# Kernel optimization log

Measured on AMD Instinct MI355X. Metric: run time of the kernel, lower is better.

## Reference

```python
import jax, jax.numpy as jnp
import numpy as np

WIN = (2, 4, 4)
SHIFT = (1, 2, 2)
NUM_HEADS = 8
LN_EPS = 1e-5


def _rel_pos_index(ws):
    wt, wh, ww = ws
    coords = np.stack(np.meshgrid(np.arange(wt), np.arange(wh), np.arange(ww), indexing='ij'))
    cf = coords.reshape(3, -1)                      # [3, N]
    rel = cf[:, :, None] - cf[:, None, :]           # [3, N, N]
    rel = rel.transpose(1, 2, 0).copy()             # [N, N, 3]
    rel[..., 0] += wt - 1
    rel[..., 1] += wh - 1
    rel[..., 2] += ww - 1
    rel[..., 0] *= (2 * wh - 1) * (2 * ww - 1)
    rel[..., 1] *= 2 * ww - 1
    return rel.sum(-1)                              # [N, N] int

REL_IDX = _rel_pos_index(WIN)


def _layer_norm(x, w, b):
    mu = jnp.mean(x, axis=-1, keepdims=True)
    var = jnp.mean(jnp.square(x - mu), axis=-1, keepdims=True)
    return (x - mu) * jax.lax.rsqrt(var + LN_EPS) * w + b


def setup_inputs() -> dict:
    key = jax.random.key(0)
    ks = jax.random.split(key, 8)
    C, Cm = 256, 1024
    inp = {
        'x': jax.random.normal(ks[0], (2, 16, 64, 64, C), jnp.float32),
        'norm1_w': jnp.ones((C,), jnp.float32),
        'norm1_b': jnp.zeros((C,), jnp.float32),
        'qkv_w': jax.random.normal(ks[1], (C, 3 * C), jnp.float32) * 0.02,
        'qkv_b': jnp.zeros((3 * C,), jnp.float32),
        'proj_w': jax.random.normal(ks[2], (C, C), jnp.float32) * 0.02,
        'proj_b': jnp.zeros((C,), jnp.float32),
        'rel_bias_table': jax.random.normal(ks[3], (147, NUM_HEADS), jnp.float32) * 0.02,
        'norm2_w': jnp.ones((C,), jnp.float32),
        'norm2_b': jnp.zeros((C,), jnp.float32),
        'mlp_w1': jax.random.normal(ks[4], (C, Cm), jnp.float32) * 0.02,
        'mlp_b1': jnp.zeros((Cm,), jnp.float32),
        'mlp_w2': jax.random.normal(ks[5], (Cm, C), jnp.float32) * 0.02,
        'mlp_b2': jnp.zeros((C,), jnp.float32),
    }
    return inp


def reference(x, norm1_w, norm1_b, qkv_w, qkv_b, proj_w, proj_b,
              rel_bias_table, norm2_w, norm2_b, mlp_w1, mlp_b1, mlp_w2, mlp_b2):
    B, T, H, W, C = x.shape
    wT, wH, wW = WIN
    nh = NUM_HEADS
    d = C // nh
    scale = d ** (-0.5)
    N = wT * wH * wW

    shortcut = x
    h = _layer_norm(x, norm1_w, norm1_b)
    # cyclic shift (no attention mask is applied in the original block)
    h = jnp.roll(h, shift=(-SHIFT[0], -SHIFT[1], -SHIFT[2]), axis=(1, 2, 3))
    # window partition -> [B*nW, N, C]
    h = h.reshape(B, T // wT, wT, H // wH, wH, W // wW, wW, C)
    h = h.transpose(0, 1, 3, 5, 2, 4, 6, 7).reshape(-1, N, C)
    B_ = h.shape[0]

    qkv = (h @ qkv_w + qkv_b).reshape(B_, N, 3, nh, d).transpose(2, 0, 3, 1, 4)
    q, k, v = qkv[0] * scale, qkv[1], qkv[2]          # [B_, nh, N, d]
    attn = jnp.einsum('bhnd,bhmd->bhnm', q, k)        # [B_, nh, N, N]
    bias = rel_bias_table[REL_IDX].transpose(2, 0, 1)  # [nh, N, N]
    attn = jax.nn.softmax(attn + bias[None], axis=-1)
    o = jnp.einsum('bhnm,bhmd->bhnd', attn, v)
    o = o.transpose(0, 2, 1, 3).reshape(B_, N, C)
    o = o @ proj_w + proj_b

    # window reverse -> [B, T, H, W, C]
    o = o.reshape(B, T // wT, H // wH, W // wW, wT, wH, wW, C)
    o = o.transpose(0, 1, 4, 2, 5, 3, 6, 7).reshape(B, T, H, W, C)
    o = jnp.roll(o, shift=SHIFT, axis=(1, 2, 3))

    x = shortcut + o
    m = _layer_norm(x, norm2_w, norm2_b)
    m = jax.nn.gelu(m @ mlp_w1 + mlp_b1, approximate=False) @ mlp_w2 + mlp_b2
    return x + m
```

## Files before the change

kernel.cpp:

```cpp
#include <hip/hip_runtime.h>
#include <hip/hip_bf16.h>
#include <cstdint>
#include <cstddef>

typedef __attribute__((ext_vector_type(8)))  short  s16x8;
typedef __attribute__((ext_vector_type(4)))  float  fp32x4;
typedef __attribute__((ext_vector_type(16))) float  fp32x16;
typedef __attribute__((ext_vector_type(4)))  unsigned short u16x4;

static __device__ __forceinline__ unsigned short f2bf(float f) {
    __hip_bfloat16 h = __float2bfloat16(f);
    return __builtin_bit_cast(unsigned short, h);
}

static __device__ __forceinline__ fp32x16 mfma32(s16x8 a, s16x8 b, fp32x16 c) {
    return __builtin_amdgcn_mfma_f32_32x32x16_bf16(a, b, c, 0, 0, 0);
}
static __device__ __forceinline__ fp32x4 mfma16(s16x8 a, s16x8 b, fp32x4 c) {
    return __builtin_amdgcn_mfma_f32_16x16x32_bf16(a, b, c, 0, 0, 0);
}

static __device__ __forceinline__ float wave_sum(float v) {
#pragma unroll
    for (int off = 32; off > 0; off >>= 1) v += __shfl_xor(v, off, 64);
    return v;
}

static __device__ __forceinline__ float gelu_f(float u) {
    float t = u * (1.0f + 0.044715f * u * u) * 1.595769122f;
    return u * (1.0f / (1.0f + __expf(-t)));
}

#define NTOK   131072
#define CDIM   256

__global__ void prep_kernel(const float* __restrict__ qkv_w, const float* __restrict__ proj_w,
                            const float* __restrict__ w1,    const float* __restrict__ w2,
                            const float* __restrict__ rel,
                            unsigned short* __restrict__ qkvT, unsigned short* __restrict__ projT,
                            unsigned short* __restrict__ w1T,  unsigned short* __restrict__ w2T,
                            float* __restrict__ btab) {
    int id = blockIdx.x * 256 + threadIdx.x;
    if (id < 196608) {
        int n = id >> 8, k = id & 255;
        qkvT[id] = f2bf(qkv_w[k * 768 + n]);
    } else if (id < 262144) {
        int e = id - 196608; int n = e >> 8, k = e & 255;
        projT[e] = f2bf(proj_w[k * 256 + n]);
    } else if (id < 524288) {
        int e = id - 262144; int n = e >> 8, k = e & 255;
        w1T[e] = f2bf(w1[k * 1024 + n]);
    } else if (id < 786432) {
        int e = id - 524288; int n = e >> 10, k = e & 1023;
        w2T[e] = f2bf(w2[k * 256 + n]);
    } else {
        int e = id - 786432;
        int h = e >> 10, rem = e & 1023, n = rem >> 5, m = rem & 31;
        int tn = n >> 4, hn = (n >> 2) & 3, wn = n & 3;
        int tm = m >> 4, hm = (m >> 2) & 3, wm = m & 3;
        int ridx = (tn - tm + 1) * 49 + (hn - hm + 3) * 7 + (wn - wm + 3);
        btab[e] = rel[ridx * 8 + h];
    }
}

__global__ __launch_bounds__(256) void ln_kernel(const float* __restrict__ in,
                                                 const float* __restrict__ w,
                                                 const float* __restrict__ b,
                                                 unsigned short* __restrict__ out) {
    int tid = threadIdx.x, lane = tid & 63, wid = tid >> 6;
    long r = (long)blockIdx.x * 4 + wid;
    int n = (int)(r & 31); int win = (int)(r >> 5);
    int b_ = win >> 11, tw = (win >> 8) & 7, hw = (win >> 4) & 15, ww = win & 15;
    int ti = n >> 4, hi = (n >> 2) & 3, wi = n & 3;
    int t = tw * 2 + ti, hh = hw * 4 + hi, wv = ww * 4 + wi;
    int ts = (t + 1) & 15, hs = (hh + 2) & 63, wsd = (wv + 2) & 63;
    long src = ((long)((b_ * 16 + ts) * 64 + hs)) * 64 + wsd;

    float4 v = *(const float4*)&in[src * CDIM + lane * 4];
    float vv[4] = {v.x, v.y, v.z, v.w};
    float s = vv[0] + vv[1] + vv[2] + vv[3];
    s = wave_sum(s);
    float mean = s * (1.0f / 256.0f);
    float q = vv[0]*vv[0] + vv[1]*vv[1] + vv[2]*vv[2] + vv[3]*vv[3];
    q = wave_sum(q);
    float var = q * (1.0f / 256.0f) - mean * mean;
    float rstd = rsqrtf(var + 1e-5f);
    int c0 = lane * 4;
    u16x4 o;
#pragma unroll
    for (int j = 0; j < 4; ++j)
        o[j] = f2bf((vv[j] - mean) * rstd * w[c0 + j] + b[c0 + j]);
    *(u16x4*)&out[r * CDIM + c0] = o;
}

template <int K, int EPI, int NS, int NX>
__global__ __launch_bounds__(256, 2) void gemm128(const unsigned short* __restrict__ A,
                                                  const unsigned short* __restrict__ Bt,
                                                  const float* __restrict__ bias,
                                                  float* __restrict__ outf,
                                                  unsigned short* __restrict__ outb) {
    __shared__ unsigned short lds[32768];
    const int tid = threadIdx.x;
    const int lane = tid & 63, wid = tid >> 6;
    const int wm = wid >> 1, wn = wid & 1;
    constexpr int NWG = 1024 * NX;
    constexpr int CPX = NWG / 8;
    const int bid = blockIdx.x;
    const int wg = (bid & 7) * CPX + (bid >> 3);
    const int n0 = (wg % NX) * 128;
    const size_t m0 = (size_t)(wg / NX) * 128;
    constexpr int NK = K / 64;

    fp32x4 acc[4][4] = {};

    const unsigned short* gA[4];
    const unsigned short* gB[4];
    int ldst[4];
#pragma unroll
    for (int i = 0; i < 4; ++i) {
        int L = i * 256 + tid;
        int r = L >> 3, c = L & 7;
        int sc = c ^ (r & 7);
        gA[i] = A  + (m0 + r) * (size_t)K + sc * 8;
        gB[i] = Bt + (size_t)(n0 + r) * K + sc * 8;
        ldst[i] = L * 8;
    }
    auto stage = [&](int buf) {
#pragma unroll
        for (int i = 0; i < 4; ++i) {
            __builtin_amdgcn_global_load_lds(
                (const __attribute__((address_space(1))) void*)gA[i],
                (__attribute__((address_space(3))) void*)(lds + buf * 16384 + ldst[i]),
                16, 0, 0);
            __builtin_amdgcn_global_load_lds(
                (const __attribute__((address_space(1))) void*)gB[i],
                (__attribute__((address_space(3))) void*)(lds + buf * 16384 + 8192 + ldst[i]),
                16, 0, 0);
            gA[i] += 64; gB[i] += 64;
        }
    };

    const int r7 = (lane & 15) & 7;
    const int aoff = (wm * 64 + (lane & 15)) * 64 + (((lane >> 4) ^ r7) << 3);
    const int boff = 8192 + (wn * 64 + (lane & 15)) * 64 + (((lane >> 4) ^ r7) << 3);

    stage(0);
    for (int kt = 0; kt < NK; ++kt) {
        __syncthreads();
        if (kt + 1 < NK) stage((kt + 1) & 1);
        const int cb = (kt & 1) * 16384;
#pragma unroll
        for (int ks = 0; ks < 2; ++ks) {
            const int kx = ks * 32;
            s16x8 a[4], b[4];
#pragma unroll
            for (int m = 0; m < 4; ++m)
                a[m] = *(const s16x8*)(lds + cb + (aoff ^ kx) + m * 1024);
#pragma unroll
            for (int n = 0; n < 4; ++n)
                b[n] = *(const s16x8*)(lds + cb + (boff ^ kx) + n * 1024);
#pragma unroll
            for (int m = 0; m < 4; ++m)
#pragma unroll
                for (int n = 0; n < 4; ++n)
                    acc[m][n] = mfma16(a[m], b[n], acc[m][n]);
        }
    }

    float bv[4];
#pragma unroll
    for (int n = 0; n < 4; ++n) bv[n] = bias[n0 + wn * 64 + n * 16 + (lane & 15)];

#pragma unroll
    for (int m = 0; m < 4; ++m) {
#pragma unroll
        for (int rg = 0; rg < 4; ++rg) {
            size_t gr = m0 + wm * 64 + m * 16 + ((lane >> 4) << 2) + rg;
#pragma unroll
            for (int n = 0; n < 4; ++n) {
                int gc = n0 + wn * 64 + n * 16 + (lane & 15);
                float v = acc[m][n][rg] + bv[n];
                if (EPI == 0) {
                    outb[gr * NS + gc] = f2bf(v);
                } else if (EPI == 2) {
                    outb[gr * NS + gc] = f2bf(gelu_f(v));
                } else {
                    outf[gr * NS + gc] += v;
                }
            }
        }
    }
}

template <int K>
__global__ __launch_bounds__(512) void gemm256_proj(const unsigned short* __restrict__ A,
                                                    const unsigned short* __restrict__ Bt,
                                                    const float* __restrict__ bias,
                                                    float* __restrict__ outf,
                                                    unsigned short* __restrict__ outb,
                                                    const float* __restrict__ resid,
                                                    const float* __restrict__ lnw,
                                                    const float* __restrict__ lnb) {
    extern __shared__ unsigned short lds[];
    const int tid = threadIdx.x;
    const int lane = tid & 63, wid = tid >> 6;
    const int wm = wid >> 2, wn = wid & 3;
    const int bid = blockIdx.x;
    const int wg = (bid & 7) * 64 + (bid >> 3);
    const size_t m0 = (size_t)wg * 256;
    constexpr int NK = K / 64;

    fp32x4 acc[8][4] = {};

    auto stage = [&](int kt, int buf) {
#pragma unroll
        for (int i = 0; i < 4; ++i) {
            int L = i * 512 + tid;
            int r = L >> 3, c = L & 7;
            int sc = c ^ (r & 7);
            const unsigned short* ga = A + (m0 + r) * K + kt * 64 + sc * 8;
            __builtin_amdgcn_global_load_lds(
                (const __attribute__((address_space(1))) void*)ga,
                (__attribute__((address_space(3))) void*)(lds + buf * 16384 + L * 8),
                16, 0, 0);
            const unsigned short* gb = Bt + (size_t)r * K + kt * 64 + sc * 8;
            __builtin_amdgcn_global_load_lds(
                (const __attribute__((address_space(1))) void*)gb,
                (__attribute__((address_space(3))) void*)(lds + 32768 + buf * 16384 + L * 8),
                16, 0, 0);
        }
    };

    stage(0, 0);
    for (int kt = 0; kt < NK; ++kt) {
        __syncthreads();
        if (kt + 1 < NK) stage(kt + 1, (kt + 1) & 1);
        const unsigned short* As = lds + (kt & 1) * 16384;
        const unsigned short* Bs = lds + 32768 + (kt & 1) * 16384;
#pragma unroll
        for (int q = 0; q < 4; ++q) {
            const int qm = q >> 1, qn = q & 1;
            s16x8 a[4][2], b[2][2];
#pragma unroll
            for (int m = 0; m < 4; ++m)
#pragma unroll
                for (int ks = 0; ks < 2; ++ks) {
                    int row = wm * 128 + qm * 64 + m * 16 + (lane & 15);
                    int j = ks * 4 + (lane >> 4);
                    a[m][ks] = *(const s16x8*)(As + row * 64 + ((j ^ (row & 7)) << 3));
                }
#pragma unroll
            for (int n = 0; n < 2; ++n)
#pragma unroll
                for (int ks = 0; ks < 2; ++ks) {
                    int row = wn * 64 + qn * 32 + n * 16 + (lane & 15);
                    int j = ks * 4 + (lane >> 4);
                    b[n][ks] = *(const s16x8*)(Bs + row * 64 + ((j ^ (row & 7)) << 3));
                }
#pragma unroll
            for (int ks = 0; ks < 2; ++ks)
#pragma unroll
                for (int m = 0; m < 4; ++m)
#pragma unroll
                    for (int n = 0; n < 2; ++n)
                        acc[qm * 4 + m][qn * 2 + n] =
                            mfma16(a[m][ks], b[n][ks], acc[qm * 4 + m][qn * 2 + n]);
        }
        __syncthreads();
    }

    float bv[4];
#pragma unroll
    for (int n = 0; n < 4; ++n) bv[n] = bias[wn * 64 + n * 16 + (lane & 15)];

    float* part = (float*)lds;
    float lw[4], lb[4];
#pragma unroll
    for (int n = 0; n < 4; ++n) {
        int gc = wn * 64 + n * 16 + (lane & 15);
        lw[n] = lnw[gc]; lb[n] = lnb[gc];
    }
#pragma unroll
    for (int m = 0; m < 8; ++m) {
#pragma unroll
        for (int rg = 0; rg < 4; ++rg) {
            int row_t = wm * 128 + m * 16 + ((lane >> 4) << 2) + rg;
            size_t gr = m0 + row_t;
            int win = (int)(gr >> 5), n_ = (int)(gr & 31);
            int b_ = win >> 11, tw = (win >> 8) & 7, hw = (win >> 4) & 15, ww = win & 15;
            int ti = n_ >> 4, hi = (n_ >> 2) & 3, wi = n_ & 3;
            int t = tw * 2 + ti, hh = hw * 4 + hi, wv = ww * 4 + wi;
            int ts = (t + 1) & 15, hs = (hh + 2) & 63, wsd = (wv + 2) & 63;
            size_t dst = ((size_t)((b_ * 16 + ts) * 64 + hs)) * 64 + wsd;
            float s = 0.f, q = 0.f;
#pragma unroll
            for (int n = 0; n < 4; ++n) {
                int gc = wn * 64 + n * 16 + (lane & 15);
                float v = acc[m][n][rg] + bv[n] + resid[dst * CDIM + gc];
                outf[dst * CDIM + gc] = v;
                acc[m][n][rg] = v;
                s += v; q += v * v;
            }
#pragma unroll
            for (int off = 1; off < 16; off <<= 1) {
                s += __shfl_xor(s, off, 16);
                q += __shfl_xor(q, off, 16);
            }
            if ((lane & 15) == 0) {
                part[(row_t * 4 + wn) * 2]     = s;
                part[(row_t * 4 + wn) * 2 + 1] = q;
            }
        }
    }
    __syncthreads();
#pragma unroll
    for (int m = 0; m < 8; ++m) {
#pragma unroll
        for (int rg = 0; rg < 4; ++rg) {
            int row_t = wm * 128 + m * 16 + ((lane >> 4) << 2) + rg;
            size_t gr = m0 + row_t;
            int win = (int)(gr >> 5), n_ = (int)(gr & 31);
            int b_ = win >> 11, tw = (win >> 8) & 7, hw = (win >> 4) & 15, ww = win & 15;
            int ti = n_ >> 4, hi = (n_ >> 2) & 3, wi = n_ & 3;
            int t = tw * 2 + ti, hh = hw * 4 + hi, wv = ww * 4 + wi;
            int ts = (t + 1) & 15, hs = (hh + 2) & 63, wsd = (wv + 2) & 63;
            size_t dst = ((size_t)((b_ * 16 + ts) * 64 + hs)) * 64 + wsd;
            float4 p0 = *(const float4*)&part[row_t * 8];
            float4 p1 = *(const float4*)&part[row_t * 8 + 4];
            float s = p0.x + p0.z + p1.x + p1.z;
            float q = p0.y + p0.w + p1.y + p1.w;
            float mean = s * (1.0f / 256.0f);
            float var  = q * (1.0f / 256.0f) - mean * mean;
            float rstd = rsqrtf(var + 1e-5f);
#pragma unroll
            for (int n = 0; n < 4; ++n) {
                int gc = wn * 64 + n * 16 + (lane & 15);
                float v = acc[m][n][rg];
                outb[dst * CDIM + gc] = f2bf((v - mean) * rstd * lw[n] + lb[n]);
            }
        }
    }
}

__global__ __launch_bounds__(256) void attn_kernel(const unsigned short* __restrict__ qkv,
                                                   const float* __restrict__ btab,
                                                   unsigned short* __restrict__ obuf) {
    __shared__ unsigned short sP[4][1280];
    __shared__ unsigned short sVt[4][1280];
    int tid = threadIdx.x, lane = tid & 63, wid = tid >> 6;
    int task = blockIdx.x * 4 + wid;
    int win = task >> 3, hh = task & 7;
    const unsigned short* base = qkv + (size_t)win * 32 * 768 + hh * 32;
    int q = lane & 31, h = lane >> 5;

    s16x8 v0 = *(const s16x8*)(base + 512 + q * 768 + h * 16);
    s16x8 v1 = *(const s16x8*)(base + 512 + q * 768 + h * 16 + 8);
#pragma unroll
    for (int j = 0; j < 8; ++j) {
        sVt[wid][(h * 16 + j) * 40 + q]     = (unsigned short)v0[j];
        sVt[wid][(h * 16 + 8 + j) * 40 + q] = (unsigned short)v1[j];
    }

    s16x8 aq0 = *(const s16x8*)(base + q * 768 + h * 8);
    s16x8 aq1 = *(const s16x8*)(base + q * 768 + 16 + h * 8);
    s16x8 bk0 = *(const s16x8*)(base + 256 + q * 768 + h * 8);
    s16x8 bk1 = *(const s16x8*)(base + 256 + q * 768 + 16 + h * 8);
    fp32x16 S = {0.0f};
    S = mfma32(aq0, bk0, S);
    S = mfma32(aq1, bk1, S);

    const float scale = 0.17677669529663687f;
    float pr[16];
#pragma unroll
    for (int r = 0; r < 16; ++r) {
        int row = (r & 3) + 8 * (r >> 2) + 4 * h;
        pr[r] = S[r] * scale + btab[(hh * 32 + row) * 32 + q];
    }
#pragma unroll
    for (int r = 0; r < 16; ++r) {
        float mx = pr[r];
#pragma unroll
        for (int off = 16; off > 0; off >>= 1) mx = fmaxf(mx, __shfl_xor(mx, off, 64));
        float e = __expf(pr[r] - mx);
        float sm = e;
#pragma unroll
        for (int off = 16; off > 0; off >>= 1) sm += __shfl_xor(sm, off, 64);
        pr[r] = e * __builtin_amdgcn_rcpf(sm);
    }
#pragma unroll
    for (int r = 0; r < 16; ++r) {
        int row = (r & 3) + 8 * (r >> 2) + 4 * h;
        sP[wid][row * 40 + q] = f2bf(pr[r]);
    }
    __syncthreads();

    s16x8 pa0 = *(const s16x8*)&sP[wid][q * 40 + h * 8];
    s16x8 pa1 = *(const s16x8*)&sP[wid][q * 40 + 16 + h * 8];
    s16x8 vb0 = *(const s16x8*)&sVt[wid][q * 40 + h * 8];
    s16x8 vb1 = *(const s16x8*)&sVt[wid][q * 40 + 16 + h * 8];
    fp32x16 O = {0.0f};
    O = mfma32(pa0, vb0, O);
    O = mfma32(pa1, vb1, O);
#pragma unroll
    for (int r = 0; r < 16; ++r) {
        int row = (r & 3) + 8 * (r >> 2) + 4 * h;
        obuf[((size_t)win * 32 + row) * 256 + hh * 32 + q] = f2bf(O[r]);
    }
}

extern "C" void kernel_launch(void* const* d_in, const int* in_sizes, int n_in,
                              void* d_out, int out_size, void* d_ws, size_t ws_size,
                              hipStream_t stream) {
    const float* x      = (const float*)d_in[0];
    const float* n1w    = (const float*)d_in[1];
    const float* n1b    = (const float*)d_in[2];
    const float* qkv_w  = (const float*)d_in[3];
    const float* qkv_b  = (const float*)d_in[4];
    const float* proj_w = (const float*)d_in[5];
    const float* proj_b = (const float*)d_in[6];
    const float* rel    = (const float*)d_in[7];
    const float* n2w    = (const float*)d_in[8];
    const float* n2b    = (const float*)d_in[9];
    const float* w1     = (const float*)d_in[10];
    const float* b1     = (const float*)d_in[11];
    const float* w2     = (const float*)d_in[12];
    const float* b2     = (const float*)d_in[13];
    float* out = (float*)d_out;

    char* ws = (char*)d_ws;
    unsigned short* hwin = (unsigned short*)ws;
    unsigned short* big  = (unsigned short*)(ws + 67108864);
    unsigned short* obuf = big + 100663296;
    char* wreg = ws + 67108864 + 268435456;
    unsigned short* qkvT  = (unsigned short*)(wreg);
    unsigned short* projT = (unsigned short*)(wreg + 393216);
    unsigned short* w1T   = (unsigned short*)(wreg + 524288);
    unsigned short* w2T   = (unsigned short*)(wreg + 1048576);
    float*          btab  = (float*)(wreg + 1572864);

    prep_kernel<<<3104, 256, 0, stream>>>(qkv_w, proj_w, w1, w2, rel, qkvT, projT, w1T, w2T, btab);

    ln_kernel<<<NTOK / 4, 256, 0, stream>>>(x, n1w, n1b, hwin);

    gemm128<256, 0, 768, 6><<<6144, 256, 0, stream>>>(hwin, qkvT, qkv_b, nullptr, big);

    attn_kernel<<<8192, 256, 0, stream>>>(big, btab, obuf);

    gemm256_proj<256><<<512, 512, 131072, stream>>>(obuf, projT, proj_b, out, hwin, x, n2w, n2b);

    gemm128<256, 2, 1024, 8><<<8192, 256, 0, stream>>>(hwin, w1T, b1, nullptr, big);

    gemm128<1024, 3, 256, 2><<<2048, 256, 0, stream>>>(big, w2T, b2, out, nullptr);
}
```

Measured before the change: 685.4 us.

## Shrink gemm128 K-tile to 32 and halve LDS to raise occupancy

The 128x128 bf16 GEMM now stages K-slices of 32 instead of 64, which halves the double-buffered LDS footprint to 32 KB. It raises the launch-bounds occupancy hint from 2 to 4 blocks per CU. The LDS swizzle is replaced with a rotation-based scheme sized for 4 chunks per row, and the K loop is fully unrolled. In exchange there are twice as many barriers and stage issues per unit of K, with less MFMA work between each sync, and register pressure must fit the tighter occupancy bound.

```diff
diff --git a/kernel.cpp b/kernel.cpp
--- a/kernel.cpp
+++ b/kernel.cpp
@@ -94,12 +94,12 @@
 }
 
 template <int K, int EPI, int NS, int NX>
-__global__ __launch_bounds__(256, 2) void gemm128(const unsigned short* __restrict__ A,
+__global__ __launch_bounds__(256, 4) void gemm128(const unsigned short* __restrict__ A,
                                                   const unsigned short* __restrict__ Bt,
                                                   const float* __restrict__ bias,
                                                   float* __restrict__ outf,
                                                   unsigned short* __restrict__ outb) {
-    __shared__ unsigned short lds[32768];
+    __shared__ unsigned short lds[16384];
     const int tid = threadIdx.x;
     const int lane = tid & 63, wid = tid >> 6;
     const int wm = wid >> 1, wn = wid & 1;
@@ -109,67 +109,71 @@
     const int wg = (bid & 7) * CPX + (bid >> 3);
     const int n0 = (wg % NX) * 128;
     const size_t m0 = (size_t)(wg / NX) * 128;
-    constexpr int NK = K / 64;
+    constexpr int NK = K / 32;
 
     fp32x4 acc[4][4] = {};
 
-    const unsigned short* gA[4];
-    const unsigned short* gB[4];
-    int ldst[4];
-#pragma unroll
-    for (int i = 0; i < 4; ++i) {
+    const unsigned short* gAp[2];
+    const unsigned short* gBp[2];
+    int dOff[2];
+#pragma unroll
+    for (int i = 0; i < 2; ++i) {
         int L = i * 256 + tid;
-        int r = L >> 3, c = L & 7;
-        int sc = c ^ (r & 7);
-        gA[i] = A  + (m0 + r) * (size_t)K + sc * 8;
-        gB[i] = Bt + (size_t)(n0 + r) * K + sc * 8;
-        ldst[i] = L * 8;
-    }
-    auto stage = [&](int buf) {
-#pragma unroll
-        for (int i = 0; i < 4; ++i) {
-            __builtin_amdgcn_global_load_lds(
-                (const __attribute__((address_space(1))) void*)gA[i],
-                (__attribute__((address_space(3))) void*)(lds + buf * 16384 + ldst[i]),
-                16, 0, 0);
-            __builtin_amdgcn_global_load_lds(
-                (const __attribute__((address_space(1))) void*)gB[i],
-                (__attribute__((address_space(3))) void*)(lds + buf * 16384 + 8192 + ldst[i]),
-                16, 0, 0);
-            gA[i] += 64; gB[i] += 64;
-        }
-    };
-
-    const int r7 = (lane & 15) & 7;
-    const int aoff = (wm * 64 + (lane & 15)) * 64 + (((lane >> 4) ^ r7) << 3);
-    const int boff = 8192 + (wn * 64 + (lane & 15)) * 64 + (((lane >> 4) ^ r7) << 3);
-
-    stage(0);
+        int r = L >> 2, cp = L & 3;
+        int j = (cp - (r >> 1)) & 3;
+        gAp[i] = A  + (m0 + r) * (size_t)K + j * 8;
+        gBp[i] = Bt + (size_t)(n0 + r) * K + j * 8;
+        dOff[i] = L * 8;
+    }
+
+    const int l15 = lane & 15, jj = lane >> 4;
+    const int sig = (jj + (l15 >> 1)) & 3;
+    const int aread = (wm * 64 + l15) * 32 + sig * 8;
+    const int bread = 4096 + (wn * 64 + l15) * 32 + sig * 8;
+
+#pragma unroll
+    for (int i = 0; i < 2; ++i) {
+        __builtin_amdgcn_global_load_lds(
+            (const __attribute__((address_space(1))) void*)gAp[i],
+            (__attribute__((address_space(3))) void*)(lds + dOff[i]), 16, 0, 0);
+        __builtin_amdgcn_global_load_lds(
+            (const __attribute__((address_space(1))) void*)gBp[i],
+            (__attribute__((address_space(3))) void*)(lds + 4096 + dOff[i]), 16, 0, 0);
+    }
+
+#pragma unroll
     for (int kt = 0; kt < NK; ++kt) {
         __syncthreads();
-        if (kt + 1 < NK) stage((kt + 1) & 1);
-        const int cb = (kt & 1) * 16384;
-#pragma unroll
-        for (int ks = 0; ks < 2; ++ks) {
-            const int kx = ks * 32;
-            s16x8 a[4], b[4];
-#pragma unroll
-            for (int m = 0; m < 4; ++m)
-                a[m] = *(const s16x8*)(lds + cb + (aoff ^ kx) + m * 1024);
+        if (kt + 1 < NK) {
+            const int nb = ((kt + 1) & 1) * 8192;
+#pragma unroll
+            for (int i = 0; i < 2; ++i) {
+                __builtin_amdgcn_global_load_lds(
+                    (const __attribute__((address_space(1))) void*)(gAp[i] + (kt + 1) * 32),
+                    (__attribute__((address_space(3))) void*)(lds + nb + dOff[i]), 16, 0, 0);
+                __builtin_amdgcn_global_load_lds(
+                    (const __attribute__((address_space(1))) void*)(gBp[i] + (kt + 1) * 32),
+                    (__attribute__((address_space(3))) void*)(lds + nb + 4096 + dOff[i]), 16, 0, 0);
+            }
+        }
+        const unsigned short* base = lds + (kt & 1) * 8192;
+        s16x8 a[4], b[4];
+#pragma unroll
+        for (int m = 0; m < 4; ++m)
+            a[m] = *(const s16x8*)(base + aread + m * 512);
+#pragma unroll
+        for (int n = 0; n < 4; ++n)
+            b[n] = *(const s16x8*)(base + bread + n * 512);
+#pragma unroll
+        for (int m = 0; m < 4; ++m)
 #pragma unroll
             for (int n = 0; n < 4; ++n)
-                b[n] = *(const s16x8*)(lds + cb + (boff ^ kx) + n * 1024);
-#pragma unroll
-            for (int m = 0; m < 4; ++m)
-#pragma unroll
-                for (int n = 0; n < 4; ++n)
-                    acc[m][n] = mfma16(a[m], b[n], acc[m][n]);
-        }
+                acc[m][n] = mfma16(a[m], b[n], acc[m][n]);
     }
 
     float bv[4];
 #pragma unroll
-    for (int n = 0; n < 4; ++n) bv[n] = bias[n0 + wn * 64 + n * 16 + (lane & 15)];
+    for (int n = 0; n < 4; ++n) bv[n] = bias[n0 + wn * 64 + n * 16 + l15];
 
 #pragma unroll
     for (int m = 0; m < 4; ++m) {
@@ -178,7 +182,7 @@
             size_t gr = m0 + wm * 64 + m * 16 + ((lane >> 4) << 2) + rg;
 #pragma unroll
             for (int n = 0; n < 4; ++n) {
-                int gc = n0 + wn * 64 + n * 16 + (lane & 15);
+                int gc = n0 + wn * 64 + n * 16 + l15;
                 float v = acc[m][n][rg] + bv[n];
                 if (EPI == 0) {
                     outb[gr * NS + gc] = f2bf(v);
```

After: 750.9 us. 1.1x slower.

## Replace 128x128 GEMM tiles with 256x256 tiles using eight waves

Applied to the files above, without the earlier changes.

Replaces the 128x128, 4-wave GEMM kernel used for the QKV, MLP1 and MLP2 projections with a 256x256, 8-wave variant that stages 128 KB of dynamic LDS with double buffering. Each wave now computes a 128x64 subtile in four quadrants. The aim is to raise arithmetic intensity and cut global and L2 traffic per FLOP. In exchange, occupancy drops to one large workgroup per CU, the workgroup count falls (512 for MLP2), and there are fewer blocks to hide latency and balance load.

```diff
diff --git a/kernel.cpp b/kernel.cpp
--- a/kernel.cpp
+++ b/kernel.cpp
@@ -94,77 +94,80 @@
 }
 
 template <int K, int EPI, int NS, int NX>
-__global__ __launch_bounds__(256, 2) void gemm128(const unsigned short* __restrict__ A,
-                                                  const unsigned short* __restrict__ Bt,
-                                                  const float* __restrict__ bias,
-                                                  float* __restrict__ outf,
-                                                  unsigned short* __restrict__ outb) {
-    __shared__ unsigned short lds[32768];
+__global__ __launch_bounds__(512) void gemm256(const unsigned short* __restrict__ A,
+                                               const unsigned short* __restrict__ Bt,
+                                               const float* __restrict__ bias,
+                                               float* __restrict__ outf,
+                                               unsigned short* __restrict__ outb) {
+    extern __shared__ unsigned short lds[];
     const int tid = threadIdx.x;
     const int lane = tid & 63, wid = tid >> 6;
-    const int wm = wid >> 1, wn = wid & 1;
-    constexpr int NWG = 1024 * NX;
+    const int wm = wid >> 2, wn = wid & 3;
+    constexpr int NWG = NX * 512;
     constexpr int CPX = NWG / 8;
     const int bid = blockIdx.x;
     const int wg = (bid & 7) * CPX + (bid >> 3);
-    const int n0 = (wg % NX) * 128;
-    const size_t m0 = (size_t)(wg / NX) * 128;
+    const int n0 = (wg % NX) * 256;
+    const size_t m0 = (size_t)(wg / NX) * 256;
     constexpr int NK = K / 64;
 
-    fp32x4 acc[4][4] = {};
-
-    const unsigned short* gA[4];
-    const unsigned short* gB[4];
-    int ldst[4];
-#pragma unroll
-    for (int i = 0; i < 4; ++i) {
-        int L = i * 256 + tid;
-        int r = L >> 3, c = L & 7;
-        int sc = c ^ (r & 7);
-        gA[i] = A  + (m0 + r) * (size_t)K + sc * 8;
-        gB[i] = Bt + (size_t)(n0 + r) * K + sc * 8;
-        ldst[i] = L * 8;
-    }
-    auto stage = [&](int buf) {
+    fp32x4 acc[8][4] = {};
+
+    auto stage = [&](int kt, int buf) {
 #pragma unroll
         for (int i = 0; i < 4; ++i) {
+            int L = i * 512 + tid;
+            int r = L >> 3, c = L & 7;
+            int sc = c ^ (r & 7);
+            const unsigned short* ga = A + (m0 + r) * K + kt * 64 + sc * 8;
             __builtin_amdgcn_global_load_lds(
-                (const __attribute__((address_space(1))) void*)gA[i],
-                (__attribute__((address_space(3))) void*)(lds + buf * 16384 + ldst[i]),
+                (const __attribute__((address_space(1))) void*)ga,
+                (__attribute__((address_space(3))) void*)(lds + buf * 16384 + L * 8),
                 16, 0, 0);
+            const unsigned short* gb = Bt + (size_t)(n0 + r) * K + kt * 64 + sc * 8;
             __builtin_amdgcn_global_load_lds(
-                (const __attribute__((address_space(1))) void*)gB[i],
-                (__attribute__((address_space(3))) void*)(lds + buf * 16384 + 8192 + ldst[i]),
+                (const __attribute__((address_space(1))) void*)gb,
+                (__attribute__((address_space(3))) void*)(lds + 32768 + buf * 16384 + L * 8),
                 16, 0, 0);
-            gA[i] += 64; gB[i] += 64;
         }
     };
 
-    const int r7 = (lane & 15) & 7;
-    const int aoff = (wm * 64 + (lane & 15)) * 64 + (((lane >> 4) ^ r7) << 3);
-    const int boff = 8192 + (wn * 64 + (lane & 15)) * 64 + (((lane >> 4) ^ r7) << 3);
-
-    stage(0);
+    stage(0, 0);
+    __syncthreads();
     for (int kt = 0; kt < NK; ++kt) {
+        if (kt + 1 < NK) stage(kt + 1, (kt + 1) & 1);
+        const unsigned short* As = lds + (kt & 1) * 16384;
+        const unsigned short* Bs = lds + 32768 + (kt & 1) * 16384;
+#pragma unroll
+        for (int q = 0; q < 4; ++q) {
+            const int qm = q >> 1, qn = q & 1;
+            s16x8 a[4][2], b[2][2];
+#pragma unroll
+            for (int m = 0; m < 4; ++m)
+#pragma unroll
+                for (int ks = 0; ks < 2; ++ks) {
+                    int row = wm * 128 + qm * 64 + m * 16 + (lane & 15);
+                    int j = ks * 4 + (lane >> 4);
+                    a[m][ks] = *(const s16x8*)(As + row * 64 + ((j ^ (row & 7)) << 3));
+                }
+#pragma unroll
+            for (int n = 0; n < 2; ++n)
+#pragma unroll
+                for (int ks = 0; ks < 2; ++ks) {
+                    int row = wn * 64 + qn * 32 + n * 16 + (lane & 15);
+                    int j = ks * 4 + (lane >> 4);
+                    b[n][ks] = *(const s16x8*)(Bs + row * 64 + ((j ^ (row & 7)) << 3));
+                }
+#pragma unroll
+            for (int ks = 0; ks < 2; ++ks)
+#pragma unroll
+                for (int m = 0; m < 4; ++m)
+#pragma unroll
+                    for (int n = 0; n < 2; ++n)
+                        acc[qm * 4 + m][qn * 2 + n] =
+                            mfma16(a[m][ks], b[n][ks], acc[qm * 4 + m][qn * 2 + n]);
+        }
         __syncthreads();
-        if (kt + 1 < NK) stage((kt + 1) & 1);
-        const int cb = (kt & 1) * 16384;
-#pragma unroll
-        for (int ks = 0; ks < 2; ++ks) {
-            const int kx = ks * 32;
-            s16x8 a[4], b[4];
-#pragma unroll
-            for (int m = 0; m < 4; ++m)
-                a[m] = *(const s16x8*)(lds + cb + (aoff ^ kx) + m * 1024);
-#pragma unroll
-            for (int n = 0; n < 4; ++n)
-                b[n] = *(const s16x8*)(lds + cb + (boff ^ kx) + n * 1024);
-#pragma unroll
-            for (int m = 0; m < 4; ++m)
-#pragma unroll
-                for (int n = 0; n < 4; ++n)
-                    acc[m][n] = mfma16(a[m], b[n], acc[m][n]);
-        }
     }
 
     float bv[4];
@@ -172,10 +175,11 @@
     for (int n = 0; n < 4; ++n) bv[n] = bias[n0 + wn * 64 + n * 16 + (lane & 15)];
 
 #pragma unroll
-    for (int m = 0; m < 4; ++m) {
+    for (int m = 0; m < 8; ++m) {
 #pragma unroll
         for (int rg = 0; rg < 4; ++rg) {
-            size_t gr = m0 + wm * 64 + m * 16 + ((lane >> 4) << 2) + rg;
+            int row_t = wm * 128 + m * 16 + ((lane >> 4) << 2) + rg;
+            size_t gr = m0 + row_t;
 #pragma unroll
             for (int n = 0; n < 4; ++n) {
                 int gc = n0 + wn * 64 + n * 16 + (lane & 15);
@@ -442,13 +446,13 @@
 
     ln_kernel<<<NTOK / 4, 256, 0, stream>>>(x, n1w, n1b, hwin);
 
-    gemm128<256, 0, 768, 6><<<6144, 256, 0, stream>>>(hwin, qkvT, qkv_b, nullptr, big);
+    gemm256<256, 0, 768, 3><<<1536, 512, 131072, stream>>>(hwin, qkvT, qkv_b, nullptr, big);
 
     attn_kernel<<<8192, 256, 0, stream>>>(big, btab, obuf);
 
     gemm256_proj<256><<<512, 512, 131072, stream>>>(obuf, projT, proj_b, out, hwin, x, n2w, n2b);
 
-    gemm128<256, 2, 1024, 8><<<8192, 256, 0, stream>>>(hwin, w1T, b1, nullptr, big);
-
-    gemm128<1024, 3, 256, 2><<<2048, 256, 0, stream>>>(big, w2T, b2, out, nullptr);
-}
+    gemm256<256, 2, 1024, 4><<<2048, 512, 131072, stream>>>(hwin, w1T, b1, nullptr, big);
+
+    gemm256<1024, 3, 256, 1><<<512, 512, 131072, stream>>>(big, w2T, b2, out, nullptr);
+}
```

New measurement: 657.0 us. -4.1%, faster.
